# Optimization experiments

Measured on AMD Instinct MI355X. Metric: run time of the kernel, lower is better.

## Reference

```python
import jax, jax.numpy as jnp
import numpy as np

B, N, H, G, WIN, MH = 8, 8192, 128, 16, 3, 16
EPS = 1e-8


def _edges(n, w):
    # local sequence edges: i -> j for j in [i-w, i+w], j != i, 0 <= j < n
    i = np.arange(n)
    off = np.concatenate([np.arange(-w, 0), np.arange(1, w + 1)])
    j = i[:, None] + off[None, :]
    m = (j >= 0) & (j < n)
    src = np.broadcast_to(i[:, None], j.shape)[m]
    dst = j[m]
    return jnp.asarray(src, jnp.int32), jnp.asarray(dst, jnp.int32)


def setup_inputs() -> dict:
    key = jax.random.key(0)
    ks = jax.random.split(key, 10)
    d = {}
    d['x_scalar'] = jax.random.normal(ks[0], (B, N, H), jnp.float32)
    d['vec'] = jax.random.normal(ks[1], (B, N, 3, H), jnp.float32)
    d['W_geom'] = jax.random.normal(ks[2], (H, G), jnp.float32) / np.sqrt(H).astype(np.float32)
    d['q_w1'] = jax.random.normal(ks[3], (2, MH), jnp.float32) * 0.5
    d['q_b1'] = jnp.zeros((MH,), jnp.float32)
    d['q_w2'] = jax.random.normal(ks[4], (MH, 1), jnp.float32) * 0.25
    d['q_b2'] = jnp.zeros((1,), jnp.float32)
    d['k_w1'] = jax.random.normal(ks[5], (2, MH), jnp.float32) * 0.5
    d['k_b1'] = jnp.zeros((MH,), jnp.float32)
    d['k_w2'] = jax.random.normal(ks[6], (MH, 1), jnp.float32) * 0.25
    d['k_b2'] = jnp.zeros((1,), jnp.float32)
    d['Wq'] = jax.random.normal(ks[7], (G, H), jnp.float32) / np.sqrt(G).astype(np.float32)
    d['bq'] = jnp.zeros((H,), jnp.float32)
    d['Wk'] = jax.random.normal(ks[8], (G, H), jnp.float32) / np.sqrt(G).astype(np.float32)
    d['bk'] = jnp.zeros((H,), jnp.float32)
    return d


def _mlp(f, w1, b1, w2, b2):
    # f: (B,E,G,2) -> (B,E,G)
    return (jax.nn.silu(f @ w1 + b1) @ w2 + b2)[..., 0]


def reference(x_scalar, vec, W_geom, q_w1, q_b1, q_w2, q_b2,
              k_w1, k_b1, k_w2, k_b2, Wq, bq, Wk, bk):
    b, n, h = x_scalar.shape
    src, dst = _edges(n, WIN)
    # project vectors into geometry subspace: (B,N,3,G)
    vec_geom = jnp.einsum('bnch,hg->bncg', vec, W_geom)
    v_i = vec_geom[:, src]          # (B,E,3,G)
    v_j = vec_geom[:, dst]
    b_ij = v_j - v_i
    norm_b = jnp.maximum(jnp.linalg.norm(b_ij, axis=2, keepdims=True), EPS)
    e_ij = b_ij / norm_b            # unit edge directions (B,E,3,G)
    # scatter-add edge directions back to source nodes: (B,N,3,G)
    u = jnp.zeros((b, n, 3, G), x_scalar.dtype).at[:, src].add(e_ij)
    u_i = u[:, src]
    u_j = u[:, dst]
    dot_ui_e = (u_i * e_ij).sum(axis=2)                       # (B,E,G)
    norm_ui = jnp.maximum(jnp.linalg.norm(u_i, axis=2), EPS)
    ang_ij = jnp.clip(dot_ui_e / norm_ui, -1.0, 1.0)
    u_i_perp = u_i - dot_ui_e[:, :, None, :] * e_ij
    dot_uj_e = (u_j * e_ij).sum(axis=2)
    u_j_perp = u_j - dot_uj_e[:, :, None, :] * e_ij
    dot_perp = (u_i_perp * u_j_perp).sum(axis=2)
    np_i = jnp.maximum(jnp.linalg.norm(u_i_perp, axis=2), EPS)
    np_j = jnp.maximum(jnp.linalg.norm(u_j_perp, axis=2), EPS)
    dih_cos = jnp.clip(dot_perp / jnp.maximum(np_i * np_j, EPS), -1.0, 1.0)
    feats = jnp.stack([ang_ij, dih_cos], axis=-1)             # (B,E,G,2)
    g_geom_q = _mlp(feats, q_w1, q_b1, q_w2, q_b2)            # (B,E,G)
    g_geom_k = _mlp(feats, k_w1, k_b1, k_w2, k_b2)
    g_q = jax.nn.sigmoid(g_geom_q @ Wq + bq)                  # (B,E,H)
    g_k = jax.nn.sigmoid(g_geom_k @ Wk + bk)
    s_j = x_scalar[:, dst]                                    # (B,E,H)
    q = jnp.zeros_like(x_scalar).at[:, src].add(g_q * s_j)
    k = jnp.zeros_like(x_scalar).at[:, src].add(g_k * s_j)
    return q, k
```

## Files before the change

kernel.cpp:

```cpp
#include <hip/hip_runtime.h>

constexpr int NB = 8;
constexpr int NN = 8192;
constexpr int NH = 128;
constexpr int NG = 16;
constexpr int NT = 36;
constexpr int NT1 = NT + 1;

typedef short s16x8 __attribute__((ext_vector_type(8)));
typedef float f32x4 __attribute__((ext_vector_type(4)));

__device__ __forceinline__ float frcp(float x) { return __builtin_amdgcn_rcpf(x); }
__device__ __forceinline__ float frsq(float x) { return __builtin_amdgcn_rsqf(x); }
__device__ __forceinline__ float fsigmoid(float x) { return frcp(1.f + __expf(-x)); }
__device__ __forceinline__ float fsilu(float x) { return x * fsigmoid(x); }
__device__ __forceinline__ float fclamp1(float x) { return fminf(fmaxf(x, -1.f), 1.f); }

__device__ __forceinline__ unsigned short f2bf(float x) {
    unsigned u = __builtin_bit_cast(unsigned, x);
    return (unsigned short)((u + 0x7FFFu + ((u >> 16) & 1u)) >> 16);
}
__device__ __forceinline__ unsigned packh2(float a, float b) {
    unsigned short lo = __builtin_bit_cast(unsigned short, (__fp16)a);
    unsigned short hi = __builtin_bit_cast(unsigned short, (__fp16)b);
    return (unsigned)lo | ((unsigned)hi << 16);
}
__device__ __forceinline__ float h2lo(unsigned u) {
    return (float)__builtin_bit_cast(__fp16, (unsigned short)(u & 0xFFFFu));
}
__device__ __forceinline__ float h2hi(unsigned u) {
    return (float)__builtin_bit_cast(__fp16, (unsigned short)(u >> 16));
}

__global__ __launch_bounds__(256) void k_table(
    const float* __restrict__ qw1, const float* __restrict__ qb1,
    const float* __restrict__ qw2, const float* __restrict__ qb2,
    const float* __restrict__ kw1, const float* __restrict__ kb1,
    const float* __restrict__ kw2, const float* __restrict__ kb2,
    unsigned* __restrict__ T) {
    int idx = blockIdx.x * 256 + threadIdx.x;
    if (idx >= NT1 * NT1) return;
    int ia = idx / NT1, id = idx % NT1;
    float a = -1.f + (float)ia * (2.f / NT);
    float d = -1.f + (float)id * (2.f / NT);
    float fq = qb2[0], fk = kb2[0];
#pragma unroll
    for (int m = 0; m < 16; ++m) {
        float hq = fmaf(a, qw1[m], fmaf(d, qw1[16 + m], qb1[m]));
        float hk = fmaf(a, kw1[m], fmaf(d, kw1[16 + m], kb1[m]));
        fq = fmaf(fsilu(hq), qw2[m], fq);
        fk = fmaf(fsilu(hk), kw2[m], fk);
    }
    T[idx] = packh2(fq, fk);
}

__global__ __launch_bounds__(256) void k_vecgeom(const float* __restrict__ vec,
                                                 const float* __restrict__ Wg,
                                                 float* __restrict__ vg) {
    __shared__ float Wl[NH * NG];
    for (int t = threadIdx.x; t < NH * NG; t += 256) Wl[t] = Wg[t];
    __syncthreads();

    int idx = blockIdx.x * 256 + threadIdx.x;
    int gq = idx & 3;
    int rc = idx >> 2;
    const float4* vrow = reinterpret_cast<const float4*>(vec + rc * NH);
    float a0 = 0.f, a1 = 0.f, a2 = 0.f, a3 = 0.f;
#pragma unroll 8
    for (int h4 = 0; h4 < 32; ++h4) {
        float4 v = vrow[h4];
        int h = h4 * 4;
        float4 w0 = *reinterpret_cast<const float4*>(&Wl[(h + 0) * NG + gq * 4]);
        float4 w1 = *reinterpret_cast<const float4*>(&Wl[(h + 1) * NG + gq * 4]);
        float4 w2 = *reinterpret_cast<const float4*>(&Wl[(h + 2) * NG + gq * 4]);
        float4 w3 = *reinterpret_cast<const float4*>(&Wl[(h + 3) * NG + gq * 4]);
        a0 = fmaf(v.x, w0.x, a0); a1 = fmaf(v.x, w0.y, a1); a2 = fmaf(v.x, w0.z, a2); a3 = fmaf(v.x, w0.w, a3);
        a0 = fmaf(v.y, w1.x, a0); a1 = fmaf(v.y, w1.y, a1); a2 = fmaf(v.y, w1.z, a2); a3 = fmaf(v.y, w1.w, a3);
        a0 = fmaf(v.z, w2.x, a0); a1 = fmaf(v.z, w2.y, a1); a2 = fmaf(v.z, w2.z, a2); a3 = fmaf(v.z, w2.w, a3);
        a0 = fmaf(v.w, w3.x, a0); a1 = fmaf(v.w, w3.y, a1); a2 = fmaf(v.w, w3.z, a2); a3 = fmaf(v.w, w3.w, a3);
    }
    *reinterpret_cast<float4*>(vg + rc * NG + gq * 4) = make_float4(a0, a1, a2, a3);
}

__global__ __launch_bounds__(256) void k_u(const float* __restrict__ vg,
                                           float* __restrict__ u) {
    int idx = blockIdx.x * 256 + threadIdx.x;
    int g = idx & 15;
    int bn = idx >> 4;
    int n = bn & (NN - 1);
    int base_i = bn * 48 + g;
    float vi0 = vg[base_i], vi1 = vg[base_i + 16], vi2 = vg[base_i + 32];
    float a0 = 0.f, a1 = 0.f, a2 = 0.f;
#pragma unroll
    for (int e = 0; e < 6; ++e) {
        int off = (e < 3) ? (e - 3) : (e - 2);
        int j = n + off;
        if (j < 0 || j >= NN) continue;
        int base_j = base_i + off * 48;
        float d0 = vg[base_j] - vi0;
        float d1 = vg[base_j + 16] - vi1;
        float d2 = vg[base_j + 32] - vi2;
        float r = frsq(fmaxf(d0 * d0 + d1 * d1 + d2 * d2, 1e-16f));
        a0 = fmaf(d0, r, a0); a1 = fmaf(d1, r, a1); a2 = fmaf(d2, r, a2);
    }
    u[base_i] = a0; u[base_i + 16] = a1; u[base_i + 32] = a2;
}

template <bool INT>
__device__ __forceinline__ void run_group(
    int bn0, int n0, int w, int lane,
    const float* __restrict__ vg, const float* __restrict__ u,
    const float* __restrict__ xs, const unsigned (&Ts)[NT1 * NT1],
    unsigned short (&As)[4][2][6][16][16], const s16x8 (&Wl)[2][8][32],
    const float (&bs)[2][NH],
    float* __restrict__ outq, float* __restrict__ outk) {

    int nl = lane >> 4, g = lane & 15;

#pragma unroll
    for (int nq = 0; nq < 4; ++nq) {
        int node = nq * 4 + nl;
        int bn = bn0 + node;
        int base_i = bn * 48 + g;
        float vi0 = vg[base_i], vi1 = vg[base_i + 16], vi2 = vg[base_i + 32];
        float ui0 = u[base_i],  ui1 = u[base_i + 16],  ui2 = u[base_i + 32];
        float rnui = frsq(fmaxf(ui0 * ui0 + ui1 * ui1 + ui2 * ui2, 1e-16f));
#pragma unroll
        for (int e = 0; e < 6; ++e) {
            int off = (e < 3) ? (e - 3) : (e - 2);
            bool valid = INT || ((unsigned)(n0 + node + off) < (unsigned)NN);
            float fq = 0.f, fk = 0.f;
            if (valid) {
                int base_j = base_i + off * 48;
                float d0 = vg[base_j] - vi0;
                float d1 = vg[base_j + 16] - vi1;
                float d2 = vg[base_j + 32] - vi2;
                float rb = frsq(fmaxf(d0 * d0 + d1 * d1 + d2 * d2, 1e-16f));
                float e0 = d0 * rb, e1 = d1 * rb, e2 = d2 * rb;
                float uj0 = u[base_j], uj1 = u[base_j + 16], uj2 = u[base_j + 32];
                float die = ui0 * e0 + ui1 * e1 + ui2 * e2;
                float ang = fclamp1(die * rnui);
                float p0 = ui0 - die * e0, p1 = ui1 - die * e1, p2 = ui2 - die * e2;
                float dje = uj0 * e0 + uj1 * e1 + uj2 * e2;
                float q0 = uj0 - dje * e0, q1 = uj1 - dje * e1, q2 = uj2 - dje * e2;
                float dp = p0 * q0 + p1 * q1 + p2 * q2;
                float pp = fmaxf(p0 * p0 + p1 * p1 + p2 * p2, 1e-16f);
                float qq = fmaxf(q0 * q0 + q1 * q1 + q2 * q2, 1e-16f);
                float dih = fclamp1(dp * frsq(pp * qq));

                float af = fmaf(ang, (float)NT * 0.5f, (float)NT * 0.5f);
                float df_ = fmaf(dih, (float)NT * 0.5f, (float)NT * 0.5f);
                int ia = min((int)af, NT - 1);
                int id = min((int)df_, NT - 1);
                float fa = af - (float)ia;
                float fd = df_ - (float)id;
                const unsigned* t0 = &Ts[ia * NT1 + id];
                unsigned c00 = t0[0], c01 = t0[1], c10 = t0[NT1], c11 = t0[NT1 + 1];
                float l0q = fmaf(fd, h2lo(c01) - h2lo(c00), h2lo(c00));
                float h0q = fmaf(fd, h2lo(c11) - h2lo(c10), h2lo(c10));
                fq = fmaf(fa, h0q - l0q, l0q);
                float l0k = fmaf(fd, h2hi(c01) - h2hi(c00), h2hi(c00));
                float h0k = fmaf(fd, h2hi(c11) - h2hi(c10), h2hi(c10));
                fk = fmaf(fa, h0k - l0k, l0k);
            }
            As[w][0][e][node][g] = f2bf(fq);
            As[w][1][e][node][g] = f2bf(fk);
        }
    }
    asm volatile("" ::: "memory");

    s16x8 afr[2][6];
    int aidx = (lane & 15) * 2 + (lane >> 4);
#pragma unroll
    for (int qk = 0; qk < 2; ++qk)
#pragma unroll
        for (int e = 0; e < 6; ++e)
            afr[qk][e] = (lane < 32)
                ? reinterpret_cast<const s16x8*>(&As[w][qk][e][0][0])[aidx]
                : (s16x8)0;

    int c = lane & 15;
    int rg = lane >> 4;
    f32x4 zero4 = {0.f, 0.f, 0.f, 0.f};

#pragma unroll
    for (int ht = 0; ht < 8; ++ht) {
        float xr[10];
#pragma unroll
        for (int d = 0; d < 10; ++d) {
            if (INT) {
                xr[d] = xs[(size_t)(bn0 + rg * 4 + d - 3) * NH + ht * 16 + c];
            } else {
                int gidx = bn0 + rg * 4 + d - 3;
                gidx = min(max(gidx, 0), NB * NN - 1);
                xr[d] = xs[(size_t)gidx * NH + ht * 16 + c];
            }
        }
#pragma unroll
        for (int qk = 0; qk < 2; ++qk) {
            s16x8 bfr = (lane < 32) ? Wl[qk][ht][lane] : (s16x8)0;
            float b = bs[qk][ht * 16 + c];
            f32x4 acc = zero4;
#pragma unroll
            for (int e = 0; e < 6; ++e) {
                f32x4 cc = __builtin_amdgcn_mfma_f32_16x16x32_bf16(afr[qk][e], bfr, zero4, 0, 0, 0);
                int off = (e < 3) ? (e - 3) : (e - 2);
#pragma unroll
                for (int r = 0; r < 4; ++r) {
                    float pr = fsigmoid(cc[r] + b);
                    if (!INT) {
                        int jn = n0 + rg * 4 + r + off;
                        pr = ((unsigned)jn < (unsigned)NN) ? pr : 0.f;
                    }
                    acc[r] = fmaf(pr, xr[r + off + 3], acc[r]);
                }
            }
            float* o = (qk ? outk : outq) + (size_t)(bn0 + rg * 4) * NH + ht * 16 + c;
#pragma unroll
            for (int r = 0; r < 4; ++r) o[r * NH] = acc[r];
        }
    }
    asm volatile("" ::: "memory");
}

__global__ __launch_bounds__(256, 4) void k_main(
    const float* __restrict__ vg, const float* __restrict__ u,
    const float* __restrict__ xs, const unsigned* __restrict__ T,
    const float* __restrict__ Wq, const float* __restrict__ bq,
    const float* __restrict__ Wk, const float* __restrict__ bk,
    float* __restrict__ outq, float* __restrict__ outk) {
    __shared__ unsigned Ts[NT1 * NT1];
    __shared__ __align__(16) unsigned short As[4][2][6][16][16];
    __shared__ s16x8 Wl[2][8][32];
    __shared__ float bs[2][NH];

    int tid = threadIdx.x;
    for (int t = tid; t < NT1 * NT1; t += 256) Ts[t] = T[t];

    for (int slot = tid; slot < 2 * 8 * 32; slot += 256) {
        int lane_in = slot & 31;
        int frag = slot >> 5;
        int fqk = frag >> 3, fht = frag & 7;
        const float* W = fqk ? Wk : Wq;
        int k0 = (lane_in >> 4) * 8, fcol = lane_in & 15;
        s16x8 v;
#pragma unroll
        for (int i = 0; i < 8; ++i)
            v[i] = (short)f2bf(W[(k0 + i) * NH + fht * 16 + fcol]);
        Wl[fqk][fht][lane_in] = v;
    }
    if (tid < NH) bs[0][tid] = bq[tid];
    else bs[1][tid - NH] = bk[tid - NH];

    int w = tid >> 6, lane = tid & 63;
    __syncthreads();

    int grp = blockIdx.x * 4 + w;
    int bn0 = grp * 16;
    int n0 = bn0 & (NN - 1);
    bool interior = (n0 != 0) && (n0 != NN - 16);
    if (interior)
        run_group<true>(bn0, n0, w, lane, vg, u, xs, Ts, As, Wl, bs, outq, outk);
    else
        run_group<false>(bn0, n0, w, lane, vg, u, xs, Ts, As, Wl, bs, outq, outk);
}

extern "C" void kernel_launch(void* const* d_in, const int* in_sizes, int n_in,
                              void* d_out, int out_size, void* d_ws, size_t ws_size,
                              hipStream_t stream) {
    const float* xs   = (const float*)d_in[0];
    const float* vec  = (const float*)d_in[1];
    const float* Wg   = (const float*)d_in[2];
    const float* qw1  = (const float*)d_in[3];
    const float* qb1  = (const float*)d_in[4];
    const float* qw2  = (const float*)d_in[5];
    const float* qb2  = (const float*)d_in[6];
    const float* kw1  = (const float*)d_in[7];
    const float* kb1  = (const float*)d_in[8];
    const float* kw2  = (const float*)d_in[9];
    const float* kb2  = (const float*)d_in[10];
    const float* Wq   = (const float*)d_in[11];
    const float* bq   = (const float*)d_in[12];
    const float* Wk   = (const float*)d_in[13];
    const float* bk   = (const float*)d_in[14];

    float* vg = (float*)d_ws;
    float* u  = vg + (size_t)NB * NN * 3 * NG;
    unsigned* T = (unsigned*)(u + (size_t)NB * NN * 3 * NG);
    float* outq = (float*)d_out;
    float* outk = outq + (size_t)NB * NN * NH;

    k_table<<<dim3((NT1 * NT1 + 255) / 256), dim3(256), 0, stream>>>(
        qw1, qb1, qw2, qb2, kw1, kb1, kw2, kb2, T);
    k_vecgeom<<<dim3(3072), dim3(256), 0, stream>>>(vec, Wg, vg);
    k_u<<<dim3(4096), dim3(256), 0, stream>>>(vg, u);
    k_main<<<dim3(1024), dim3(256), 0, stream>>>(
        vg, u, xs, T, Wq, bq, Wk, bk, outq, outk);
}
```

Measured before the change: 81.41 us.

## Split fused main kernel into separate gate and apply kernels via workspace

Splits the fused per-group kernel into a gate-computation kernel that writes bf16 gate fragments to a workspace buffer and an apply kernel where each wave handles one of q or k. The aim is more waves in flight and lower per-wave register and LDS pressure, with launch bounds raised to 8 blocks per CU. The bias is also folded into the MFMA accumulator input. In exchange it adds an extra kernel launch and a global round trip for the gate tensor. The original fused kernel remains as a fallback when the workspace is too small.

```diff
diff --git a/kernel.cpp b/kernel.cpp
--- a/kernel.cpp
+++ b/kernel.cpp
@@ -6,6 +6,7 @@
 constexpr int NG = 16;
 constexpr int NT = 36;
 constexpr int NT1 = NT + 1;
+constexpr int NGRP = NB * NN / 16;
 
 typedef short s16x8 __attribute__((ext_vector_type(8)));
 typedef float f32x4 __attribute__((ext_vector_type(4)));
@@ -106,6 +107,181 @@
     u[base_i] = a0; u[base_i + 16] = a1; u[base_i + 32] = a2;
 }
 
+__device__ __forceinline__ void edge_gates(
+    int base_i, int base_j,
+    float vi0, float vi1, float vi2,
+    float ui0, float ui1, float ui2, float rnui,
+    const float* __restrict__ vg, const float* __restrict__ u,
+    const unsigned (&Ts)[NT1 * NT1], float& fq, float& fk) {
+    float d0 = vg[base_j] - vi0;
+    float d1 = vg[base_j + 16] - vi1;
+    float d2 = vg[base_j + 32] - vi2;
+    float rb = frsq(fmaxf(d0 * d0 + d1 * d1 + d2 * d2, 1e-16f));
+    float e0 = d0 * rb, e1 = d1 * rb, e2 = d2 * rb;
+    float uj0 = u[base_j], uj1 = u[base_j + 16], uj2 = u[base_j + 32];
+    float die = ui0 * e0 + ui1 * e1 + ui2 * e2;
+    float ang = fclamp1(die * rnui);
+    float p0 = ui0 - die * e0, p1 = ui1 - die * e1, p2 = ui2 - die * e2;
+    float dje = uj0 * e0 + uj1 * e1 + uj2 * e2;
+    float q0 = uj0 - dje * e0, q1 = uj1 - dje * e1, q2 = uj2 - dje * e2;
+    float dp = p0 * q0 + p1 * q1 + p2 * q2;
+    float pp = fmaxf(p0 * p0 + p1 * p1 + p2 * p2, 1e-16f);
+    float qq = fmaxf(q0 * q0 + q1 * q1 + q2 * q2, 1e-16f);
+    float dih = fclamp1(dp * frsq(pp * qq));
+
+    float af = fmaf(ang, (float)NT * 0.5f, (float)NT * 0.5f);
+    float df_ = fmaf(dih, (float)NT * 0.5f, (float)NT * 0.5f);
+    int ia = min((int)af, NT - 1);
+    int id = min((int)df_, NT - 1);
+    float fa = af - (float)ia;
+    float fd = df_ - (float)id;
+    const unsigned* t0 = &Ts[ia * NT1 + id];
+    unsigned c00 = t0[0], c01 = t0[1], c10 = t0[NT1], c11 = t0[NT1 + 1];
+    float l0q = fmaf(fd, h2lo(c01) - h2lo(c00), h2lo(c00));
+    float h0q = fmaf(fd, h2lo(c11) - h2lo(c10), h2lo(c10));
+    fq = fmaf(fa, h0q - l0q, l0q);
+    float l0k = fmaf(fd, h2hi(c01) - h2hi(c00), h2hi(c00));
+    float h0k = fmaf(fd, h2hi(c11) - h2hi(c10), h2hi(c10));
+    fk = fmaf(fa, h0k - l0k, l0k);
+}
+
+template <bool INT>
+__device__ __forceinline__ void gates_half(
+    int grp, int bn0, int n0, int sub, int lane,
+    const float* __restrict__ vg, const float* __restrict__ u,
+    const unsigned (&Ts)[NT1 * NT1], unsigned short* __restrict__ GT) {
+    int nl = lane >> 4, g = lane & 15;
+    size_t gbase = ((size_t)grp * 12) * 256;
+#pragma unroll
+    for (int i = 0; i < 2; ++i) {
+        int nq = sub * 2 + i;
+        int node = nq * 4 + nl;
+        int bn = bn0 + node;
+        int base_i = bn * 48 + g;
+        float vi0 = vg[base_i], vi1 = vg[base_i + 16], vi2 = vg[base_i + 32];
+        float ui0 = u[base_i],  ui1 = u[base_i + 16],  ui2 = u[base_i + 32];
+        float rnui = frsq(fmaxf(ui0 * ui0 + ui1 * ui1 + ui2 * ui2, 1e-16f));
+#pragma unroll
+        for (int e = 0; e < 6; ++e) {
+            int off = (e < 3) ? (e - 3) : (e - 2);
+            bool valid = INT || ((unsigned)(n0 + node + off) < (unsigned)NN);
+            float fq = 0.f, fk = 0.f;
+            if (valid)
+                edge_gates(base_i, base_i + off * 48, vi0, vi1, vi2,
+                           ui0, ui1, ui2, rnui, vg, u, Ts, fq, fk);
+            size_t o = gbase + (size_t)e * 256 + nq * 64 + lane;
+            GT[o] = f2bf(fq);
+            GT[o + 6 * 256] = f2bf(fk);
+        }
+    }
+}
+
+__global__ __launch_bounds__(256, 8) void k_gates(
+    const float* __restrict__ vg, const float* __restrict__ u,
+    const unsigned* __restrict__ T, unsigned short* __restrict__ GT) {
+    __shared__ unsigned Ts[NT1 * NT1];
+    int tid = threadIdx.x;
+    for (int t = tid; t < NT1 * NT1; t += 256) Ts[t] = T[t];
+    __syncthreads();
+
+    int w = tid >> 6, lane = tid & 63;
+    int gw = blockIdx.x * 4 + w;
+    int grp = gw >> 1, sub = gw & 1;
+    int bn0 = grp * 16;
+    int n0 = bn0 & (NN - 1);
+    bool interior = (n0 != 0) && (n0 != NN - 16);
+    if (interior) gates_half<true>(grp, bn0, n0, sub, lane, vg, u, Ts, GT);
+    else          gates_half<false>(grp, bn0, n0, sub, lane, vg, u, Ts, GT);
+}
+
+template <bool INT>
+__device__ __forceinline__ void apply_group(
+    int grp, int bn0, int n0, int qk, int lane,
+    const unsigned short* __restrict__ GT, const float* __restrict__ xs,
+    const s16x8 (&Wl)[2][8][32], const float (&bs)[2][NH],
+    float* __restrict__ out) {
+    int c = lane & 15, rg = lane >> 4;
+    s16x8 afr[6];
+    int aidx = (lane & 15) * 2 + (lane >> 4);
+    const unsigned short* gt = GT + ((size_t)(grp * 2 + qk) * 6) * 256;
+#pragma unroll
+    for (int e = 0; e < 6; ++e)
+        afr[e] = (lane < 32)
+            ? reinterpret_cast<const s16x8*>(gt + e * 256)[aidx]
+            : (s16x8)0;
+
+#pragma unroll
+    for (int ht = 0; ht < 8; ++ht) {
+        float xr[10];
+#pragma unroll
+        for (int d = 0; d < 10; ++d) {
+            if (INT) {
+                xr[d] = xs[(size_t)(bn0 + rg * 4 + d - 3) * NH + ht * 16 + c];
+            } else {
+                int gidx = bn0 + rg * 4 + d - 3;
+                gidx = min(max(gidx, 0), NB * NN - 1);
+                xr[d] = xs[(size_t)gidx * NH + ht * 16 + c];
+            }
+        }
+        s16x8 bfr = (lane < 32) ? Wl[qk][ht][lane] : (s16x8)0;
+        float b = bs[qk][ht * 16 + c];
+        f32x4 bias4 = {b, b, b, b};
+        f32x4 acc = {0.f, 0.f, 0.f, 0.f};
+#pragma unroll
+        for (int e = 0; e < 6; ++e) {
+            f32x4 cc = __builtin_amdgcn_mfma_f32_16x16x32_bf16(afr[e], bfr, bias4, 0, 0, 0);
+            int off = (e < 3) ? (e - 3) : (e - 2);
+#pragma unroll
+            for (int r = 0; r < 4; ++r) {
+                float pr = fsigmoid(cc[r]);
+                if (!INT) {
+                    int jn = n0 + rg * 4 + r + off;
+                    pr = ((unsigned)jn < (unsigned)NN) ? pr : 0.f;
+                }
+                acc[r] = fmaf(pr, xr[r + off + 3], acc[r]);
+            }
+        }
+        float* o = out + (size_t)(bn0 + rg * 4) * NH + ht * 16 + c;
+#pragma unroll
+        for (int r = 0; r < 4; ++r) o[r * NH] = acc[r];
+    }
+}
+
+__global__ __launch_bounds__(256, 8) void k_apply(
+    const unsigned short* __restrict__ GT, const float* __restrict__ xs,
+    const float* __restrict__ Wq, const float* __restrict__ bq,
+    const float* __restrict__ Wk, const float* __restrict__ bk,
+    float* __restrict__ outq, float* __restrict__ outk) {
+    __shared__ s16x8 Wl[2][8][32];
+    __shared__ float bs[2][NH];
+    int tid = threadIdx.x;
+    for (int slot = tid; slot < 2 * 8 * 32; slot += 256) {
+        int lane_in = slot & 31;
+        int frag = slot >> 5;
+        int fqk = frag >> 3, fht = frag & 7;
+        const float* W = fqk ? Wk : Wq;
+        int k0 = (lane_in >> 4) * 8, fcol = lane_in & 15;
+        s16x8 v;
+#pragma unroll
+        for (int i = 0; i < 8; ++i)
+            v[i] = (short)f2bf(W[(k0 + i) * NH + fht * 16 + fcol]);
+        Wl[fqk][fht][lane_in] = v;
+    }
+    if (tid < NH) bs[0][tid] = bq[tid];
+    else bs[1][tid - NH] = bk[tid - NH];
+    __syncthreads();
+
+    int w = tid >> 6, lane = tid & 63;
+    int gw = blockIdx.x * 4 + w;
+    int grp = gw >> 1, qk = gw & 1;
+    int bn0 = grp * 16;
+    int n0 = bn0 & (NN - 1);
+    float* out = qk ? outk : outq;
+    bool interior = (n0 != 0) && (n0 != NN - 16);
+    if (interior) apply_group<true>(grp, bn0, n0, qk, lane, GT, xs, Wl, bs, out);
+    else          apply_group<false>(grp, bn0, n0, qk, lane, GT, xs, Wl, bs, out);
+}
+
 template <bool INT>
 __device__ __forceinline__ void run_group(
     int bn0, int n0, int w, int lane,
@@ -116,7 +292,6 @@
     float* __restrict__ outq, float* __restrict__ outk) {
 
     int nl = lane >> 4, g = lane & 15;
-
 #pragma unroll
     for (int nq = 0; nq < 4; ++nq) {
         int node = nq * 4 + nl;
@@ -130,39 +305,9 @@
             int off = (e < 3) ? (e - 3) : (e - 2);
             bool valid = INT || ((unsigned)(n0 + node + off) < (unsigned)NN);
             float fq = 0.f, fk = 0.f;
-            if (valid) {
-                int base_j = base_i + off * 48;
-                float d0 = vg[base_j] - vi0;
-                float d1 = vg[base_j + 16] - vi1;
-                float d2 = vg[base_j + 32] - vi2;
-                float rb = frsq(fmaxf(d0 * d0 + d1 * d1 + d2 * d2, 1e-16f));
-                float e0 = d0 * rb, e1 = d1 * rb, e2 = d2 * rb;
-                float uj0 = u[base_j], uj1 = u[base_j + 16], uj2 = u[base_j + 32];
-                float die = ui0 * e0 + ui1 * e1 + ui2 * e2;
-                float ang = fclamp1(die * rnui);
-                float p0 = ui0 - die * e0, p1 = ui1 - die * e1, p2 = ui2 - die * e2;
-                float dje = uj0 * e0 + uj1 * e1 + uj2 * e2;
-                float q0 = uj0 - dje * e0, q1 = uj1 - dje * e1, q2 = uj2 - dje * e2;
-                float dp = p0 * q0 + p1 * q1 + p2 * q2;
-                float pp = fmaxf(p0 * p0 + p1 * p1 + p2 * p2, 1e-16f);
-                float qq = fmaxf(q0 * q0 + q1 * q1 + q2 * q2, 1e-16f);
-                float dih = fclamp1(dp * frsq(pp * qq));
-
-                float af = fmaf(ang, (float)NT * 0.5f, (float)NT * 0.5f);
-                float df_ = fmaf(dih, (float)NT * 0.5f, (float)NT * 0.5f);
-                int ia = min((int)af, NT - 1);
-                int id = min((int)df_, NT - 1);
-                float fa = af - (float)ia;
-                float fd = df_ - (float)id;
-                const unsigned* t0 = &Ts[ia * NT1 + id];
-                unsigned c00 = t0[0], c01 = t0[1], c10 = t0[NT1], c11 = t0[NT1 + 1];
-                float l0q = fmaf(fd, h2lo(c01) - h2lo(c00), h2lo(c00));
-                float h0q = fmaf(fd, h2lo(c11) - h2lo(c10), h2lo(c10));
-                fq = fmaf(fa, h0q - l0q, l0q);
-                float l0k = fmaf(fd, h2hi(c01) - h2hi(c00), h2hi(c00));
-                float h0k = fmaf(fd, h2hi(c11) - h2hi(c10), h2hi(c10));
-                fk = fmaf(fa, h0k - l0k, l0k);
-            }
+            if (valid)
+                edge_gates(base_i, base_i + off * 48, vi0, vi1, vi2,
+                           ui0, ui1, ui2, rnui, vg, u, Ts, fq, fk);
             As[w][0][e][node][g] = f2bf(fq);
             As[w][1][e][node][g] = f2bf(fk);
         }
@@ -181,8 +326,6 @@
 
     int c = lane & 15;
     int rg = lane >> 4;
-    f32x4 zero4 = {0.f, 0.f, 0.f, 0.f};
-
 #pragma unroll
     for (int ht = 0; ht < 8; ++ht) {
         float xr[10];
@@ -200,14 +343,15 @@
         for (int qk = 0; qk < 2; ++qk) {
             s16x8 bfr = (lane < 32) ? Wl[qk][ht][lane] : (s16x8)0;
             float b = bs[qk][ht * 16 + c];
-            f32x4 acc = zero4;
+            f32x4 bias4 = {b, b, b, b};
+            f32x4 acc = {0.f, 0.f, 0.f, 0.f};
 #pragma unroll
             for (int e = 0; e < 6; ++e) {
-                f32x4 cc = __builtin_amdgcn_mfma_f32_16x16x32_bf16(afr[qk][e], bfr, zero4, 0, 0, 0);
+                f32x4 cc = __builtin_amdgcn_mfma_f32_16x16x32_bf16(afr[qk][e], bfr, bias4, 0, 0, 0);
                 int off = (e < 3) ? (e - 3) : (e - 2);
 #pragma unroll
                 for (int r = 0; r < 4; ++r) {
-                    float pr = fsigmoid(cc[r] + b);
+                    float pr = fsigmoid(cc[r]);
                     if (!INT) {
                         int jn = n0 + rg * 4 + r + off;
                         pr = ((unsigned)jn < (unsigned)NN) ? pr : 0.f;
@@ -236,7 +380,6 @@
 
     int tid = threadIdx.x;
     for (int t = tid; t < NT1 * NT1; t += 256) Ts[t] = T[t];
-
     for (int slot = tid; slot < 2 * 8 * 32; slot += 256) {
         int lane_in = slot & 31;
         int frag = slot >> 5;
@@ -284,9 +427,14 @@
     const float* Wk   = (const float*)d_in[13];
     const float* bk   = (const float*)d_in[14];
 
+    size_t vg_f = (size_t)NB * NN * 48;
     float* vg = (float*)d_ws;
-    float* u  = vg + (size_t)NB * NN * 3 * NG;
-    unsigned* T = (unsigned*)(u + (size_t)NB * NN * 3 * NG);
+    float* u  = vg + vg_f;
+    unsigned* T = (unsigned*)(u + vg_f);
+    size_t t_off = 2 * vg_f * 4;
+    size_t gt_off = t_off + 8192;
+    unsigned short* GT = (unsigned short*)((char*)d_ws + gt_off);
+    size_t need = gt_off + (size_t)NGRP * 12 * 256 * 2;
     float* outq = (float*)d_out;
     float* outk = outq + (size_t)NB * NN * NH;
 
@@ -294,6 +442,13 @@
         qw1, qb1, qw2, qb2, kw1, kb1, kw2, kb2, T);
     k_vecgeom<<<dim3(3072), dim3(256), 0, stream>>>(vec, Wg, vg);
     k_u<<<dim3(4096), dim3(256), 0, stream>>>(vg, u);
-    k_main<<<dim3(1024), dim3(256), 0, stream>>>(
-        vg, u, xs, T, Wq, bq, Wk, bk, outq, outk);
-}
+
+    if (ws_size >= need) {
+        k_gates<<<dim3(2048), dim3(256), 0, stream>>>(vg, u, T, GT);
+        k_apply<<<dim3(2048), dim3(256), 0, stream>>>(
+            GT, xs, Wq, bq, Wk, bk, outq, outk);
+    } else {
+        k_main<<<dim3(1024), dim3(256), 0, stream>>>(
+            vg, u, xs, T, Wq, bq, Wk, bk, outq, outk);
+    }
+}
```

After: 129.5 us. +59.1%, slower.

## Split node groups across wave pairs for gate build and q/k projection

Applied to the files above, without the earlier changes.

Each 16-node group is now handled by two waves instead of one. Both waves build half of the edge gate features each, then sync, then one wave does the q projection and the other the k projection. The grid doubles to 2048 blocks, and the launch-bounds occupancy hint rises from 4 to 5. The bias is folded into the MFMA accumulator input. The aim is more parallelism and a shorter per-wave serial chain, at the cost of an extra block barrier and each group's x_scalar window being loaded by both waves.

```diff
diff --git a/kernel.cpp b/kernel.cpp
--- a/kernel.cpp
+++ b/kernel.cpp
@@ -106,19 +106,54 @@
     u[base_i] = a0; u[base_i + 16] = a1; u[base_i + 32] = a2;
 }
 
+__device__ __forceinline__ void edge_gates(
+    int base_i, int base_j,
+    float vi0, float vi1, float vi2,
+    float ui0, float ui1, float ui2, float rnui,
+    const float* __restrict__ vg, const float* __restrict__ u,
+    const unsigned (&Ts)[NT1 * NT1], float& fq, float& fk) {
+    float d0 = vg[base_j] - vi0;
+    float d1 = vg[base_j + 16] - vi1;
+    float d2 = vg[base_j + 32] - vi2;
+    float rb = frsq(fmaxf(d0 * d0 + d1 * d1 + d2 * d2, 1e-16f));
+    float e0 = d0 * rb, e1 = d1 * rb, e2 = d2 * rb;
+    float uj0 = u[base_j], uj1 = u[base_j + 16], uj2 = u[base_j + 32];
+    float die = ui0 * e0 + ui1 * e1 + ui2 * e2;
+    float ang = fclamp1(die * rnui);
+    float p0 = ui0 - die * e0, p1 = ui1 - die * e1, p2 = ui2 - die * e2;
+    float dje = uj0 * e0 + uj1 * e1 + uj2 * e2;
+    float q0 = uj0 - dje * e0, q1 = uj1 - dje * e1, q2 = uj2 - dje * e2;
+    float dp = p0 * q0 + p1 * q1 + p2 * q2;
+    float pp = fmaxf(p0 * p0 + p1 * p1 + p2 * p2, 1e-16f);
+    float qq = fmaxf(q0 * q0 + q1 * q1 + q2 * q2, 1e-16f);
+    float dih = fclamp1(dp * frsq(pp * qq));
+
+    float af = fmaf(ang, (float)NT * 0.5f, (float)NT * 0.5f);
+    float df_ = fmaf(dih, (float)NT * 0.5f, (float)NT * 0.5f);
+    int ia = min((int)af, NT - 1);
+    int id = min((int)df_, NT - 1);
+    float fa = af - (float)ia;
+    float fd = df_ - (float)id;
+    const unsigned* t0 = &Ts[ia * NT1 + id];
+    unsigned c00 = t0[0], c01 = t0[1], c10 = t0[NT1], c11 = t0[NT1 + 1];
+    float l0q = fmaf(fd, h2lo(c01) - h2lo(c00), h2lo(c00));
+    float h0q = fmaf(fd, h2lo(c11) - h2lo(c10), h2lo(c10));
+    fq = fmaf(fa, h0q - l0q, l0q);
+    float l0k = fmaf(fd, h2hi(c01) - h2hi(c00), h2hi(c00));
+    float h0k = fmaf(fd, h2hi(c11) - h2hi(c10), h2hi(c10));
+    fk = fmaf(fa, h0k - l0k, l0k);
+}
+
 template <bool INT>
-__device__ __forceinline__ void run_group(
-    int bn0, int n0, int w, int lane,
+__device__ __forceinline__ void phaseA(
+    int bn0, int n0, int gh, int sub, int lane,
     const float* __restrict__ vg, const float* __restrict__ u,
-    const float* __restrict__ xs, const unsigned (&Ts)[NT1 * NT1],
-    unsigned short (&As)[4][2][6][16][16], const s16x8 (&Wl)[2][8][32],
-    const float (&bs)[2][NH],
-    float* __restrict__ outq, float* __restrict__ outk) {
-
+    const unsigned (&Ts)[NT1 * NT1],
+    unsigned short (&As)[2][2][6][16][16]) {
     int nl = lane >> 4, g = lane & 15;
-
-#pragma unroll
-    for (int nq = 0; nq < 4; ++nq) {
+#pragma unroll
+    for (int i = 0; i < 2; ++i) {
+        int nq = sub * 2 + i;
         int node = nq * 4 + nl;
         int bn = bn0 + node;
         int base_i = bn * 48 + g;
@@ -130,58 +165,30 @@
             int off = (e < 3) ? (e - 3) : (e - 2);
             bool valid = INT || ((unsigned)(n0 + node + off) < (unsigned)NN);
             float fq = 0.f, fk = 0.f;
-            if (valid) {
-                int base_j = base_i + off * 48;
-                float d0 = vg[base_j] - vi0;
-                float d1 = vg[base_j + 16] - vi1;
-                float d2 = vg[base_j + 32] - vi2;
-                float rb = frsq(fmaxf(d0 * d0 + d1 * d1 + d2 * d2, 1e-16f));
-                float e0 = d0 * rb, e1 = d1 * rb, e2 = d2 * rb;
-                float uj0 = u[base_j], uj1 = u[base_j + 16], uj2 = u[base_j + 32];
-                float die = ui0 * e0 + ui1 * e1 + ui2 * e2;
-                float ang = fclamp1(die * rnui);
-                float p0 = ui0 - die * e0, p1 = ui1 - die * e1, p2 = ui2 - die * e2;
-                float dje = uj0 * e0 + uj1 * e1 + uj2 * e2;
-                float q0 = uj0 - dje * e0, q1 = uj1 - dje * e1, q2 = uj2 - dje * e2;
-                float dp = p0 * q0 + p1 * q1 + p2 * q2;
-                float pp = fmaxf(p0 * p0 + p1 * p1 + p2 * p2, 1e-16f);
-                float qq = fmaxf(q0 * q0 + q1 * q1 + q2 * q2, 1e-16f);
-                float dih = fclamp1(dp * frsq(pp * qq));
-
-                float af = fmaf(ang, (float)NT * 0.5f, (float)NT * 0.5f);
-                float df_ = fmaf(dih, (float)NT * 0.5f, (float)NT * 0.5f);
-                int ia = min((int)af, NT - 1);
-                int id = min((int)df_, NT - 1);
-                float fa = af - (float)ia;
-                float fd = df_ - (float)id;
-                const unsigned* t0 = &Ts[ia * NT1 + id];
-                unsigned c00 = t0[0], c01 = t0[1], c10 = t0[NT1], c11 = t0[NT1 + 1];
-                float l0q = fmaf(fd, h2lo(c01) - h2lo(c00), h2lo(c00));
-                float h0q = fmaf(fd, h2lo(c11) - h2lo(c10), h2lo(c10));
-                fq = fmaf(fa, h0q - l0q, l0q);
-                float l0k = fmaf(fd, h2hi(c01) - h2hi(c00), h2hi(c00));
-                float h0k = fmaf(fd, h2hi(c11) - h2hi(c10), h2hi(c10));
-                fk = fmaf(fa, h0k - l0k, l0k);
-            }
-            As[w][0][e][node][g] = f2bf(fq);
-            As[w][1][e][node][g] = f2bf(fk);
+            if (valid)
+                edge_gates(base_i, base_i + off * 48, vi0, vi1, vi2,
+                           ui0, ui1, ui2, rnui, vg, u, Ts, fq, fk);
+            As[gh][0][e][node][g] = f2bf(fq);
+            As[gh][1][e][node][g] = f2bf(fk);
         }
     }
-    asm volatile("" ::: "memory");
-
-    s16x8 afr[2][6];
-    int aidx = (lane & 15) * 2 + (lane >> 4);
-#pragma unroll
-    for (int qk = 0; qk < 2; ++qk)
-#pragma unroll
-        for (int e = 0; e < 6; ++e)
-            afr[qk][e] = (lane < 32)
-                ? reinterpret_cast<const s16x8*>(&As[w][qk][e][0][0])[aidx]
-                : (s16x8)0;
-
-    int c = lane & 15;
-    int rg = lane >> 4;
-    f32x4 zero4 = {0.f, 0.f, 0.f, 0.f};
+}
+
+template <bool INT>
+__device__ __forceinline__ void phaseB(
+    int bn0, int n0, int gh, int qk, int lane,
+    const float* __restrict__ xs,
+    const unsigned short (&As)[2][2][6][16][16],
+    const s16x8 (&Wl)[2][8][32], const float (&bs)[2][NH],
+    float* __restrict__ out) {
+    int c = lane & 15, rg = lane >> 4;
+    s16x8 afr[6];
+    int aidx = c * 2 + rg;
+#pragma unroll
+    for (int e = 0; e < 6; ++e)
+        afr[e] = (lane < 32)
+            ? reinterpret_cast<const s16x8*>(&As[gh][qk][e][0][0])[aidx]
+            : (s16x8)0;
 
 #pragma unroll
     for (int ht = 0; ht < 8; ++ht) {
@@ -196,41 +203,38 @@
                 xr[d] = xs[(size_t)gidx * NH + ht * 16 + c];
             }
         }
-#pragma unroll
-        for (int qk = 0; qk < 2; ++qk) {
-            s16x8 bfr = (lane < 32) ? Wl[qk][ht][lane] : (s16x8)0;
-            float b = bs[qk][ht * 16 + c];
-            f32x4 acc = zero4;
-#pragma unroll
-            for (int e = 0; e < 6; ++e) {
-                f32x4 cc = __builtin_amdgcn_mfma_f32_16x16x32_bf16(afr[qk][e], bfr, zero4, 0, 0, 0);
-                int off = (e < 3) ? (e - 3) : (e - 2);
-#pragma unroll
-                for (int r = 0; r < 4; ++r) {
-                    float pr = fsigmoid(cc[r] + b);
-                    if (!INT) {
-                        int jn = n0 + rg * 4 + r + off;
-                        pr = ((unsigned)jn < (unsigned)NN) ? pr : 0.f;
-                    }
-                    acc[r] = fmaf(pr, xr[r + off + 3], acc[r]);
+        s16x8 bfr = (lane < 32) ? Wl[qk][ht][lane] : (s16x8)0;
+        float b = bs[qk][ht * 16 + c];
+        f32x4 bias4 = {b, b, b, b};
+        f32x4 acc = {0.f, 0.f, 0.f, 0.f};
+#pragma unroll
+        for (int e = 0; e < 6; ++e) {
+            f32x4 cc = __builtin_amdgcn_mfma_f32_16x16x32_bf16(afr[e], bfr, bias4, 0, 0, 0);
+            int off = (e < 3) ? (e - 3) : (e - 2);
+#pragma unroll
+            for (int r = 0; r < 4; ++r) {
+                float pr = fsigmoid(cc[r]);
+                if (!INT) {
+                    int jn = n0 + rg * 4 + r + off;
+                    pr = ((unsigned)jn < (unsigned)NN) ? pr : 0.f;
                 }
+                acc[r] = fmaf(pr, xr[r + off + 3], acc[r]);
             }
-            float* o = (qk ? outk : outq) + (size_t)(bn0 + rg * 4) * NH + ht * 16 + c;
-#pragma unroll
-            for (int r = 0; r < 4; ++r) o[r * NH] = acc[r];
         }
-    }
-    asm volatile("" ::: "memory");
-}
-
-__global__ __launch_bounds__(256, 4) void k_main(
+        float* o = out + (size_t)(bn0 + rg * 4) * NH + ht * 16 + c;
+#pragma unroll
+        for (int r = 0; r < 4; ++r) o[r * NH] = acc[r];
+    }
+}
+
+__global__ __launch_bounds__(256, 5) void k_main(
     const float* __restrict__ vg, const float* __restrict__ u,
     const float* __restrict__ xs, const unsigned* __restrict__ T,
     const float* __restrict__ Wq, const float* __restrict__ bq,
     const float* __restrict__ Wk, const float* __restrict__ bk,
     float* __restrict__ outq, float* __restrict__ outk) {
     __shared__ unsigned Ts[NT1 * NT1];
-    __shared__ __align__(16) unsigned short As[4][2][6][16][16];
+    __shared__ __align__(16) unsigned short As[2][2][6][16][16];
     __shared__ s16x8 Wl[2][8][32];
     __shared__ float bs[2][NH];
 
@@ -253,16 +257,22 @@
     else bs[1][tid - NH] = bk[tid - NH];
 
     int w = tid >> 6, lane = tid & 63;
-    __syncthreads();
-
-    int grp = blockIdx.x * 4 + w;
+    int gh = w >> 1, sub = w & 1;
+    int grp = blockIdx.x * 2 + gh;
     int bn0 = grp * 16;
     int n0 = bn0 & (NN - 1);
     bool interior = (n0 != 0) && (n0 != NN - 16);
-    if (interior)
-        run_group<true>(bn0, n0, w, lane, vg, u, xs, Ts, As, Wl, bs, outq, outk);
-    else
-        run_group<false>(bn0, n0, w, lane, vg, u, xs, Ts, As, Wl, bs, outq, outk);
+
+    __syncthreads();
+
+    if (interior) phaseA<true>(bn0, n0, gh, sub, lane, vg, u, Ts, As);
+    else          phaseA<false>(bn0, n0, gh, sub, lane, vg, u, Ts, As);
+
+    __syncthreads();
+
+    float* out = sub ? outk : outq;
+    if (interior) phaseB<true>(bn0, n0, gh, sub, lane, xs, As, Wl, bs, out);
+    else          phaseB<false>(bn0, n0, gh, sub, lane, xs, As, Wl, bs, out);
 }
 
 extern "C" void kernel_launch(void* const* d_in, const int* in_sizes, int n_in,
@@ -284,9 +294,10 @@
     const float* Wk   = (const float*)d_in[13];
     const float* bk   = (const float*)d_in[14];
 
+    size_t vg_f = (size_t)NB * NN * 48;
     float* vg = (float*)d_ws;
-    float* u  = vg + (size_t)NB * NN * 3 * NG;
-    unsigned* T = (unsigned*)(u + (size_t)NB * NN * 3 * NG);
+    float* u  = vg + vg_f;
+    unsigned* T = (unsigned*)(u + vg_f);
     float* outq = (float*)d_out;
     float* outk = outq + (size_t)NB * NN * NH;
 
@@ -294,6 +305,6 @@
         qw1, qb1, qw2, qb2, kw1, kb1, kw2, kb2, T);
     k_vecgeom<<<dim3(3072), dim3(256), 0, stream>>>(vec, Wg, vg);
     k_u<<<dim3(4096), dim3(256), 0, stream>>>(vg, u);
-    k_main<<<dim3(1024), dim3(256), 0, stream>>>(
+    k_main<<<dim3(2048), dim3(256), 0, stream>>>(
         vg, u, xs, T, Wq, bq, Wk, bk, outq, outk);
 }
```

Measured after the change: 80.02 us. No clear change (-1.7%).
